# Optimization experiments

Hardware: AMD Instinct MI355X
Metric: run time of the kernel (lower is better)

Reference implementation:

```python
import jax, jax.numpy as jnp
import numpy as np

N, C, F_CAT, F_NUM, V = 250000, 32, 16, 16, 64


def setup_inputs() -> dict:
    key = jax.random.key(0)
    k0, k1, k2, k3, k4, k5 = jax.random.split(key, 6)
    X_cat = jax.random.randint(k0, (N, F_CAT), 0, V)
    X_num = jax.random.normal(k1, (N, F_NUM), dtype=jnp.float32)
    class_probs = jax.random.uniform(k2, (C,), dtype=jnp.float32)
    class_probs = class_probs / class_probs.sum()
    # conditional probs are smoothed counts/size_class in fit(); keep them positive
    cat_probs = jax.random.uniform(k3, (C, F_CAT, V), dtype=jnp.float32) * 0.9 + 0.05
    means = jax.random.normal(k4, (C, F_NUM), dtype=jnp.float32)
    stds = jax.random.uniform(k5, (C, F_NUM), dtype=jnp.float32) + 0.5  # keep away from 0
    return {"X_cat": X_cat, "X_num": X_num, "class_probs": class_probs,
            "cat_probs": cat_probs, "means": means, "stds": stds}


def reference(X_cat, X_num, class_probs, cat_probs, means, stds):
    # X_cat: [N, F_cat] int indices; X_num: [N, F_num] float
    # cat_probs: [C, F_cat, V]; means/stds: [C, F_num]; class_probs: [C]
    C_, Fc, _ = cat_probs.shape
    # categorical gather -> [N, C, F_cat]
    ci = jnp.arange(C_)[None, :, None]
    fi = jnp.arange(Fc)[None, None, :]
    gathered = cat_probs[ci, fi, X_cat[:, None, :]]
    cat_term = jnp.prod(gathered, axis=-1)            # [N, C]
    # gaussian likelihood (faithful to module: 1/(2*pi*std^2) * exp(-0.5*z^2))
    pi = jnp.float32(np.pi)
    x = X_num[:, None, :]                             # [N, 1, F_num]
    z = (x - means[None]) / stds[None]
    lik = 1.0 / (2.0 * pi * stds[None] ** 2) * jnp.exp(-0.5 * z ** 2)  # [N, C, F_num]
    num_term = jnp.prod(lik, axis=-1)                 # [N, C]
    pred_probs = class_probs[None, :] * cat_term * num_term
    return jnp.argmax(pred_probs, axis=1)
```

## Files before the change

### kernel.cpp

```cpp
#include <hip/hip_runtime.h>
#include <math.h>

constexpr int kN  = 250000;
constexpr int kC  = 32;
constexpr int kFC = 16;
constexpr int kFN = 16;
constexpr int kV  = 64;
constexpr int kBlock = 1024;

constexpr int kRowF2 = 9;

constexpr int kOffCnt  = 1056;
constexpr int kOffTab  = 1088;
constexpr int kOffB    = kOffTab + 1024 * kC;
constexpr int kOffS    = kOffB + 2 * kN;
constexpr int kOffIBdw = kOffB + 4 * kN;
constexpr int kOffList = kOffIBdw + (2 * kN + 3) / 4;
constexpr size_t kWsNeedSplit = (size_t)(kOffList + kN) * 4;


__global__ __launch_bounds__(256) void nbc_prep(
    const float* __restrict__ class_probs,
    const float* __restrict__ means,
    const float* __restrict__ stds,
    const float* __restrict__ cat_probs,
    float* __restrict__ ws,
    int use_tab)
{
    const int b = blockIdx.x;
    const int t = threadIdx.x;
    if (b == 0) {
        const float two_pi = 2.0f * (float)M_PI;
        for (int i = t; i < kC * kFN; i += 256) {
            float m  = means[i];
            float s  = stds[i];
            float rs = 1.0f / s;
            ws[2 * i]     = -0.5f * rs * rs;
            ws[2 * i + 1] = m * rs * rs;
        }
        if (t == 0) reinterpret_cast<int*>(ws)[kOffCnt] = 0;
        if (t < kC) {
            float k = logf(class_probs[t]);
            for (int f = 0; f < kFN; ++f) {
                float s  = stds[t * kFN + f];
                float m  = means[t * kFN + f];
                float rs = 1.0f / s;
                k += logf(1.0f / (two_pi * (s * s)));
                k += -0.5f * (m * rs) * (m * rs);
            }
            ws[1024 + t] = k;
        }
    } else if (use_tab) {
        const int base = (b - 1) * 1024;
        for (int k2 = 0; k2 < 4; ++k2) {
            int s = base + t + k2 * 256;
            int c = s >> 10;
            int r = s & 1023;
            ws[kOffTab + r * 32 + c] = logf(cat_probs[s]);
        }
    }
}

__global__ __launch_bounds__(kBlock) void nbc_half(
    const int*   __restrict__ X_cat,
    const float* __restrict__ X_num,
    const float* __restrict__ cat_probs,
    float* __restrict__ ws)
{
    __shared__ float2 lcat[1024 * kRowF2];

    const int chunk = blockIdx.x >> 1;
    const int half  = blockIdx.x & 1;
    const int tid   = threadIdx.x;
    const int n     = chunk * kBlock + tid;
    const bool active = (n < kN);

    unsigned pack[4];
    float    x[kFN];
    if (active) {
        const int4* p4 = reinterpret_cast<const int4*>(X_cat + (size_t)n * kFC);
        int4 a0 = p4[0], a1 = p4[1], a2 = p4[2], a3 = p4[3];
        pack[0] = (unsigned)a0.x | ((unsigned)a0.y << 8) |
                  ((unsigned)a0.z << 16) | ((unsigned)a0.w << 24);
        pack[1] = (unsigned)a1.x | ((unsigned)a1.y << 8) |
                  ((unsigned)a1.z << 16) | ((unsigned)a1.w << 24);
        pack[2] = (unsigned)a2.x | ((unsigned)a2.y << 8) |
                  ((unsigned)a2.z << 16) | ((unsigned)a2.w << 24);
        pack[3] = (unsigned)a3.x | ((unsigned)a3.y << 8) |
                  ((unsigned)a3.z << 16) | ((unsigned)a3.w << 24);

        const float4* q4 = reinterpret_cast<const float4*>(X_num + (size_t)n * kFN);
        float4 b0 = q4[0], b1 = q4[1], b2 = q4[2], b3 = q4[3];
        x[0]=b0.x;  x[1]=b0.y;  x[2]=b0.z;  x[3]=b0.w;
        x[4]=b1.x;  x[5]=b1.y;  x[6]=b1.z;  x[7]=b1.w;
        x[8]=b2.x;  x[9]=b2.y;  x[10]=b2.z; x[11]=b2.w;
        x[12]=b3.x; x[13]=b3.y; x[14]=b3.z; x[15]=b3.w;
    } else {
        pack[0] = pack[1] = pack[2] = pack[3] = 0u;
        #pragma unroll
        for (int f = 0; f < kFN; ++f) x[f] = 0.0f;
    }

    {
        #pragma unroll
        for (int q = 0; q < 4; ++q) {
            float4 w = *reinterpret_cast<const float4*>(
                ws + kOffTab + tid * 32 + (half << 4) + q * 4);
            lcat[tid * kRowF2 + q * 2]     = make_float2(w.x, w.y);
            lcat[tid * kRowF2 + q * 2 + 1] = make_float2(w.z, w.w);
        }
    }
    __syncthreads();

    if (!active) return;

    int rowf2[kFC];
    #pragma unroll
    for (int f = 0; f < kFC; ++f) {
        const int v = (pack[f >> 2] >> ((f & 3) * 8)) & 63;
        rowf2[f] = ((f << 6) + v) * kRowF2;
    }

    const float2* __restrict__ P = reinterpret_cast<const float2*>(ws);
    const float*  __restrict__ K = ws + 1024;

    float best = -INFINITY, second = -INFINITY;
    int   besti = 0;

    #pragma unroll 1
    for (int grp = 0; grp < 4; ++grp) {
        const int cbase = (half << 4) + (grp << 2);
        float acc[4];

        #pragma unroll
        for (int j = 0; j < 4; ++j) {
            const int c = cbase + j;
            float a = K[c];
            #pragma unroll
            for (int f = 0; f < kFN; ++f) {
                float2 p = P[(c << 4) + f];
                a = fmaf(x[f], fmaf(x[f], p.x, p.y), a);
            }
            acc[j] = a;
        }

        #pragma unroll
        for (int f = 0; f < kFC; ++f) {
            const float2 lo = lcat[rowf2[f] + (grp << 1)];
            const float2 hi = lcat[rowf2[f] + (grp << 1) + 1];
            acc[0] += lo.x;
            acc[1] += lo.y;
            acc[2] += hi.x;
            acc[3] += hi.y;
        }

        #pragma unroll
        for (int j = 0; j < 4; ++j) {
            float T = acc[j];
            if (T > best)        { second = best; best = T; besti = cbase + j; }
            else if (T > second) { second = T; }
        }
    }

    ws[kOffB + half * kN + n] = best;
    ws[kOffS + half * kN + n] = second;
    reinterpret_cast<unsigned char*>(ws)[(size_t)kOffIBdw * 4 + half * kN + n] =
        (unsigned char)besti;
}

__global__ __launch_bounds__(256) void nbc_merge_fast(
    float* __restrict__ ws,
    int* __restrict__ out)
{
    const int n = blockIdx.x * 256 + threadIdx.x;
    if (n >= kN) return;

    const float b0 = ws[kOffB + n];
    const float b1 = ws[kOffB + kN + n];
    const float s0 = ws[kOffS + n];
    const float s1 = ws[kOffS + kN + n];
    const unsigned char* ib =
        reinterpret_cast<const unsigned char*>(ws) + (size_t)kOffIBdw * 4;
    const int i0 = ib[n];
    const int i1 = ib[kN + n];

    float wb, ws2; int wi;
    if (b1 > b0) { wb = b1; wi = i1; ws2 = fmaxf(b0, s1); }
    else         { wb = b0; wi = i0; ws2 = fmaxf(b1, s0); }

    if (wb >= -86.0f && (wb - ws2) >= 8.0e-3f) {
        out[n] = wi;
    } else {
        int slot = atomicAdd(reinterpret_cast<int*>(ws) + kOffCnt, 1);
        reinterpret_cast<int*>(ws)[kOffList + slot] = n;
    }
}

__global__ __launch_bounds__(256) void nbc_exact(
    const int*   __restrict__ X_cat,
    const float* __restrict__ X_num,
    const float* __restrict__ class_probs,
    const float* __restrict__ cat_probs,
    const float* __restrict__ means,
    const float* __restrict__ stds,
    const float* __restrict__ ws,
    int* __restrict__ out)
{
    const int total  = reinterpret_cast<const int*>(ws)[kOffCnt];
    const int c      = threadIdx.x & 31;
    const int gid0   = (blockIdx.x * 256 + threadIdx.x) >> 5;
    const int gstride = (gridDim.x * 256) >> 5;
    const float two_pi = 2.0f * (float)M_PI;

    for (int g = gid0; g < total; g += gstride) {
        const int n = reinterpret_cast<const int*>(ws)[kOffList + g];

        unsigned pack[4];
        float    x[kFN];
        {
            const int4* p4 = reinterpret_cast<const int4*>(X_cat + (size_t)n * kFC);
            int4 a0 = p4[0], a1 = p4[1], a2 = p4[2], a3 = p4[3];
            pack[0] = (unsigned)a0.x | ((unsigned)a0.y << 8) |
                      ((unsigned)a0.z << 16) | ((unsigned)a0.w << 24);
            pack[1] = (unsigned)a1.x | ((unsigned)a1.y << 8) |
                      ((unsigned)a1.z << 16) | ((unsigned)a1.w << 24);
            pack[2] = (unsigned)a2.x | ((unsigned)a2.y << 8) |
                      ((unsigned)a2.z << 16) | ((unsigned)a2.w << 24);
            pack[3] = (unsigned)a3.x | ((unsigned)a3.y << 8) |
                      ((unsigned)a3.z << 16) | ((unsigned)a3.w << 24);

            const float4* q4 =
                reinterpret_cast<const float4*>(X_num + (size_t)n * kFN);
            float4 c0 = q4[0], c1 = q4[1], c2 = q4[2], c3 = q4[3];
            x[0]=c0.x;  x[1]=c0.y;  x[2]=c0.z;  x[3]=c0.w;
            x[4]=c1.x;  x[5]=c1.y;  x[6]=c1.z;  x[7]=c1.w;
            x[8]=c2.x;  x[9]=c2.y;  x[10]=c2.z; x[11]=c2.w;
            x[12]=c3.x; x[13]=c3.y; x[14]=c3.z; x[15]=c3.w;
        }

        const float* __restrict__ row = cat_probs + (size_t)c * (kFC * kV);
        float cat = row[pack[0] & 63];
        #pragma unroll
        for (int f = 1; f < kFC; ++f) {
            const int v = (pack[f >> 2] >> ((f & 3) * 8)) & 63;
            cat *= row[(f << 6) + v];
        }
        float num;
        #pragma unroll
        for (int f = 0; f < kFN; ++f) {
            float m = means[c * kFN + f];
            float s = stds [c * kFN + f];
            float inv = 1.0f / (two_pi * (s * s));
            float z = (x[f] - m) / s;
            float e = expf(-0.5f * (z * z));
            float lik = inv * e;
            num = (f == 0) ? lik : num * lik;
        }
        float pred = (class_probs[c] * cat) * num;

        float bb = pred;
        int   bi = c;
        #pragma unroll
        for (int m2 = 1; m2 < 32; m2 <<= 1) {
            float ov = __shfl_xor(bb, m2);
            int   oi = __shfl_xor(bi, m2);
            if (ov > bb || (ov == bb && oi < bi)) { bb = ov; bi = oi; }
        }
        if (c == 0) out[n] = bi;
    }
}

__global__ __launch_bounds__(kBlock) void nbc_mono(
    const int*   __restrict__ X_cat,
    const float* __restrict__ X_num,
    const float* __restrict__ class_probs,
    const float* __restrict__ cat_probs,
    const float* __restrict__ means,
    const float* __restrict__ stds,
    const float* __restrict__ ws,
    int* __restrict__ out)
{
    __shared__ float lcat[1024 * 36];

    const int tid = threadIdx.x;
    const int n   = blockIdx.x * kBlock + tid;
    const bool active = (n < kN);

    unsigned pack[4];
    float    x[kFN];
    if (active) {
        const int4* p4 = reinterpret_cast<const int4*>(X_cat + (size_t)n * kFC);
        int4 a0 = p4[0], a1 = p4[1], a2 = p4[2], a3 = p4[3];
        pack[0] = (unsigned)a0.x | ((unsigned)a0.y << 8) |
                  ((unsigned)a0.z << 16) | ((unsigned)a0.w << 24);
        pack[1] = (unsigned)a1.x | ((unsigned)a1.y << 8) |
                  ((unsigned)a1.z << 16) | ((unsigned)a1.w << 24);
        pack[2] = (unsigned)a2.x | ((unsigned)a2.y << 8) |
                  ((unsigned)a2.z << 16) | ((unsigned)a2.w << 24);
        pack[3] = (unsigned)a3.x | ((unsigned)a3.y << 8) |
                  ((unsigned)a3.z << 16) | ((unsigned)a3.w << 24);
        const float4* q4 = reinterpret_cast<const float4*>(X_num + (size_t)n * kFN);
        float4 b0 = q4[0], b1 = q4[1], b2 = q4[2], b3 = q4[3];
        x[0]=b0.x;  x[1]=b0.y;  x[2]=b0.z;  x[3]=b0.w;
        x[4]=b1.x;  x[5]=b1.y;  x[6]=b1.z;  x[7]=b1.w;
        x[8]=b2.x;  x[9]=b2.y;  x[10]=b2.z; x[11]=b2.w;
        x[12]=b3.x; x[13]=b3.y; x[14]=b3.z; x[15]=b3.w;
    } else {
        pack[0] = pack[1] = pack[2] = pack[3] = 0u;
        #pragma unroll
        for (int f = 0; f < kFN; ++f) x[f] = 0.0f;
    }

    #pragma unroll
    for (int cg = 0; cg < 8; ++cg) {
        float4 w;
        w.x = logf(cat_probs[(size_t)(cg * 4 + 0) * 1024 + tid]);
        w.y = logf(cat_probs[(size_t)(cg * 4 + 1) * 1024 + tid]);
        w.z = logf(cat_probs[(size_t)(cg * 4 + 2) * 1024 + tid]);
        w.w = logf(cat_probs[(size_t)(cg * 4 + 3) * 1024 + tid]);
        *reinterpret_cast<float4*>(lcat + (size_t)tid * 36 + cg * 4) = w;
    }
    __syncthreads();

    if (!active) return;

    int rowdw[kFC];
    #pragma unroll
    for (int f = 0; f < kFC; ++f) {
        const int v = (pack[f >> 2] >> ((f & 3) * 8)) & 63;
        rowdw[f] = ((f << 6) + v) * 36;
    }

    const float2* __restrict__ P = reinterpret_cast<const float2*>(ws);
    const float*  __restrict__ K = ws + 1024;

    float best = -INFINITY, second = -INFINITY;
    int   besti = 0;

    #pragma unroll 1
    for (int grp = 0; grp < 8; ++grp) {
        const int cbase = grp << 2;
        float acc[4];
        #pragma unroll
        for (int j = 0; j < 4; ++j) {
            const int c = cbase + j;
            float a = K[c];
            #pragma unroll
            for (int f = 0; f < kFN; ++f) {
                float2 p = P[(c << 4) + f];
                a = fmaf(x[f], fmaf(x[f], p.x, p.y), a);
            }
            acc[j] = a;
        }
        #pragma unroll
        for (int f = 0; f < kFC; ++f) {
            const float4 t = *reinterpret_cast<const float4*>(
                &lcat[rowdw[f] + (grp << 2)]);
            acc[0] += t.x; acc[1] += t.y; acc[2] += t.z; acc[3] += t.w;
        }
        #pragma unroll
        for (int j = 0; j < 4; ++j) {
            float T = acc[j];
            if (T > best)        { second = best; best = T; besti = cbase + j; }
            else if (T > second) { second = T; }
        }
    }

    if (best >= -86.0f && (best - second) >= 8.0e-3f) {
        out[n] = besti;
        return;
    }

    const float thr    = (best >= -86.0f) ? (best - 1.6e-2f) : -INFINITY;
    const float two_pi = 2.0f * (float)M_PI;
    float bb = -INFINITY;
    int   bi = 0;
    for (int c = 0; c < kC; ++c) {
        float a = K[c];
        #pragma unroll
        for (int f = 0; f < kFN; ++f) {
            float2 p = P[(c << 4) + f];
            a = fmaf(x[f], fmaf(x[f], p.x, p.y), a);
        }
        #pragma unroll
        for (int f = 0; f < kFC; ++f) a += lcat[rowdw[f] + c];

        if (a >= thr) {
            const float* __restrict__ row = cat_probs + (size_t)c * (kFC * kV);
            float cat = row[pack[0] & 63];
            #pragma unroll
            for (int f = 1; f < kFC; ++f) {
                const int v = (pack[f >> 2] >> ((f & 3) * 8)) & 63;
                cat *= row[(f << 6) + v];
            }
            float num;
            #pragma unroll
            for (int f = 0; f < kFN; ++f) {
                float m = means[c * kFN + f];
                float s = stds [c * kFN + f];
                float inv = 1.0f / (two_pi * (s * s));
                float z = (x[f] - m) / s;
                float e = expf(-0.5f * (z * z));
                float lik = inv * e;
                num = (f == 0) ? lik : num * lik;
            }
            float pred = (class_probs[c] * cat) * num;
            if (pred > bb) { bb = pred; bi = c; }
        }
    }
    out[n] = bi;
}

extern "C" void kernel_launch(void* const* d_in, const int* in_sizes, int n_in,
                              void* d_out, int out_size, void* d_ws, size_t ws_size,
                              hipStream_t stream) {
    const int*   X_cat       = (const int*)  d_in[0];
    const float* X_num       = (const float*)d_in[1];
    const float* class_probs = (const float*)d_in[2];
    const float* cat_probs   = (const float*)d_in[3];
    const float* means       = (const float*)d_in[4];
    const float* stds        = (const float*)d_in[5];
    int*   out = (int*)d_out;
    float* ws  = (float*)d_ws;

    const int use_tab = (ws_size >= kWsNeedSplit) ? 1 : 0;

    hipLaunchKernelGGL(nbc_prep, dim3(use_tab ? 33 : 1), dim3(256), 0, stream,
                       class_probs, means, stds, cat_probs, ws, use_tab);

    const int chunks = (kN + kBlock - 1) / kBlock;
    if (use_tab) {
        hipLaunchKernelGGL(nbc_half, dim3(chunks * 2), dim3(kBlock), 0, stream,
                           X_cat, X_num, cat_probs, ws);
        hipLaunchKernelGGL(nbc_merge_fast, dim3((kN + 255) / 256), dim3(256),
                           0, stream, ws, out);
        hipLaunchKernelGGL(nbc_exact, dim3(2048), dim3(256), 0, stream,
                           X_cat, X_num, class_probs, cat_probs, means, stds,
                           ws, out);
    } else {
        hipLaunchKernelGGL(nbc_mono, dim3(chunks), dim3(kBlock), 0, stream,
                           X_cat, X_num, class_probs, cat_probs, means, stds,
                           ws, out);
    }
}
```

Measured before the change: 131.1 us.

## Split class scoring into quarters with 512-thread blocks and smaller LDS tables

```diff
diff --git a/kernel.cpp b/kernel.cpp
--- a/kernel.cpp
+++ b/kernel.cpp
@@ -6,16 +6,16 @@
 constexpr int kFC = 16;
 constexpr int kFN = 16;
 constexpr int kV  = 64;
-constexpr int kBlock = 1024;
-
-constexpr int kRowF2 = 9;
+
+constexpr int kQBlock = 512;
+constexpr int kRowQ2  = 5;
 
 constexpr int kOffCnt  = 1056;
 constexpr int kOffTab  = 1088;
 constexpr int kOffB    = kOffTab + 1024 * kC;
-constexpr int kOffS    = kOffB + 2 * kN;
-constexpr int kOffIBdw = kOffB + 4 * kN;
-constexpr int kOffList = kOffIBdw + (2 * kN + 3) / 4;
+constexpr int kOffS    = kOffB + 4 * kN;
+constexpr int kOffIBdw = kOffS + 4 * kN;
+constexpr int kOffList = kOffIBdw + kN;
 constexpr size_t kWsNeedSplit = (size_t)(kOffList + kN) * 4;
 
 
@@ -61,18 +61,17 @@
     }
 }
 
-__global__ __launch_bounds__(kBlock) void nbc_half(
+__global__ __launch_bounds__(kQBlock) void nbc_quarter(
     const int*   __restrict__ X_cat,
     const float* __restrict__ X_num,
-    const float* __restrict__ cat_probs,
     float* __restrict__ ws)
 {
-    __shared__ float2 lcat[1024 * kRowF2];
-
-    const int chunk = blockIdx.x >> 1;
-    const int half  = blockIdx.x & 1;
-    const int tid   = threadIdx.x;
-    const int n     = chunk * kBlock + tid;
+    __shared__ float2 lcat[1024 * kRowQ2];
+
+    const int chunk   = blockIdx.x >> 2;
+    const int quarter = blockIdx.x & 3;
+    const int tid     = threadIdx.x;
+    const int n       = chunk * kQBlock + tid;
     const bool active = (n < kN);
 
     unsigned pack[4];
@@ -102,23 +101,28 @@
     }
 
     {
-        #pragma unroll
-        for (int q = 0; q < 4; ++q) {
-            float4 w = *reinterpret_cast<const float4*>(
-                ws + kOffTab + tid * 32 + (half << 4) + q * 4);
-            lcat[tid * kRowF2 + q * 2]     = make_float2(w.x, w.y);
-            lcat[tid * kRowF2 + q * 2 + 1] = make_float2(w.z, w.w);
+        const float4* __restrict__ lt4 =
+            reinterpret_cast<const float4*>(ws + kOffTab);
+        #pragma unroll
+        for (int r2 = 0; r2 < 2; ++r2) {
+            const int r = tid + r2 * kQBlock;
+            float4 w0 = lt4[r * 8 + quarter * 2];
+            float4 w1 = lt4[r * 8 + quarter * 2 + 1];
+            lcat[r * kRowQ2 + 0] = make_float2(w0.x, w0.y);
+            lcat[r * kRowQ2 + 1] = make_float2(w0.z, w0.w);
+            lcat[r * kRowQ2 + 2] = make_float2(w1.x, w1.y);
+            lcat[r * kRowQ2 + 3] = make_float2(w1.z, w1.w);
         }
     }
     __syncthreads();
 
     if (!active) return;
 
-    int rowf2[kFC];
+    int rowq[kFC];
     #pragma unroll
     for (int f = 0; f < kFC; ++f) {
         const int v = (pack[f >> 2] >> ((f & 3) * 8)) & 63;
-        rowf2[f] = ((f << 6) + v) * kRowF2;
+        rowq[f] = ((f << 6) + v) * kRowQ2;
     }
 
     const float2* __restrict__ P = reinterpret_cast<const float2*>(ws);
@@ -128,8 +132,8 @@
     int   besti = 0;
 
     #pragma unroll 1
-    for (int grp = 0; grp < 4; ++grp) {
-        const int cbase = (half << 4) + (grp << 2);
+    for (int grp = 0; grp < 2; ++grp) {
+        const int cbase = (quarter << 3) + (grp << 2);
         float acc[4];
 
         #pragma unroll
@@ -146,8 +150,8 @@
 
         #pragma unroll
         for (int f = 0; f < kFC; ++f) {
-            const float2 lo = lcat[rowf2[f] + (grp << 1)];
-            const float2 hi = lcat[rowf2[f] + (grp << 1) + 1];
+            const float2 lo = lcat[rowq[f] + (grp << 1)];
+            const float2 hi = lcat[rowq[f] + (grp << 1) + 1];
             acc[0] += lo.x;
             acc[1] += lo.y;
             acc[2] += hi.x;
@@ -162,10 +166,10 @@
         }
     }
 
-    ws[kOffB + half * kN + n] = best;
-    ws[kOffS + half * kN + n] = second;
-    reinterpret_cast<unsigned char*>(ws)[(size_t)kOffIBdw * 4 + half * kN + n] =
-        (unsigned char)besti;
+    ws[kOffB + quarter * kN + n] = best;
+    ws[kOffS + quarter * kN + n] = second;
+    reinterpret_cast<unsigned char*>(ws)[(size_t)kOffIBdw * 4 +
+                                         quarter * kN + n] = (unsigned char)besti;
 }
 
 __global__ __launch_bounds__(256) void nbc_merge_fast(
@@ -175,18 +179,20 @@
     const int n = blockIdx.x * 256 + threadIdx.x;
     if (n >= kN) return;
 
-    const float b0 = ws[kOffB + n];
-    const float b1 = ws[kOffB + kN + n];
-    const float s0 = ws[kOffS + n];
-    const float s1 = ws[kOffS + kN + n];
     const unsigned char* ib =
         reinterpret_cast<const unsigned char*>(ws) + (size_t)kOffIBdw * 4;
-    const int i0 = ib[n];
-    const int i1 = ib[kN + n];
-
-    float wb, ws2; int wi;
-    if (b1 > b0) { wb = b1; wi = i1; ws2 = fmaxf(b0, s1); }
-    else         { wb = b0; wi = i0; ws2 = fmaxf(b1, s0); }
+
+    float wb  = ws[kOffB + n];
+    float ws2 = ws[kOffS + n];
+    int   wi  = ib[n];
+    #pragma unroll
+    for (int q = 1; q < 4; ++q) {
+        const float bq = ws[kOffB + q * kN + n];
+        const float sq = ws[kOffS + q * kN + n];
+        const int   iq = ib[q * kN + n];
+        if (bq > wb) { ws2 = fmaxf(wb, sq); wb = bq; wi = iq; }
+        else         { ws2 = fmaxf(ws2, bq); }
+    }
 
     if (wb >= -86.0f && (wb - ws2) >= 8.0e-3f) {
         out[n] = wi;
@@ -270,7 +276,7 @@
     }
 }
 
-__global__ __launch_bounds__(kBlock) void nbc_mono(
+__global__ __launch_bounds__(1024) void nbc_mono(
     const int*   __restrict__ X_cat,
     const float* __restrict__ X_num,
     const float* __restrict__ class_probs,
@@ -283,7 +289,7 @@
     __shared__ float lcat[1024 * 36];
 
     const int tid = threadIdx.x;
-    const int n   = blockIdx.x * kBlock + tid;
+    const int n   = blockIdx.x * 1024 + tid;
     const bool active = (n < kN);
 
     unsigned pack[4];
@@ -428,17 +434,18 @@
     hipLaunchKernelGGL(nbc_prep, dim3(use_tab ? 33 : 1), dim3(256), 0, stream,
                        class_probs, means, stds, cat_probs, ws, use_tab);
 
-    const int chunks = (kN + kBlock - 1) / kBlock;
     if (use_tab) {
-        hipLaunchKernelGGL(nbc_half, dim3(chunks * 2), dim3(kBlock), 0, stream,
-                           X_cat, X_num, cat_probs, ws);
+        const int chunks512 = (kN + kQBlock - 1) / kQBlock;
+        hipLaunchKernelGGL(nbc_quarter, dim3(chunks512 * 4), dim3(kQBlock),
+                           0, stream, X_cat, X_num, ws);
         hipLaunchKernelGGL(nbc_merge_fast, dim3((kN + 255) / 256), dim3(256),
                            0, stream, ws, out);
         hipLaunchKernelGGL(nbc_exact, dim3(2048), dim3(256), 0, stream,
                            X_cat, X_num, class_probs, cat_probs, means, stds,
                            ws, out);
     } else {
-        hipLaunchKernelGGL(nbc_mono, dim3(chunks), dim3(kBlock), 0, stream,
+        const int chunks1024 = (kN + 1023) / 1024;
+        hipLaunchKernelGGL(nbc_mono, dim3(chunks1024), dim3(1024), 0, stream,
                            X_cat, X_num, class_probs, cat_probs, means, stds,
                            ws, out);
     }
```

After: 133.6 us. Within noise of the previous version (+1.9%).
